# Performance work log

Measured on AMD Instinct MI355X. Metric: run time of the kernel, lower is better.

Reference implementation:

```python
import jax, jax.numpy as jnp
import numpy as np

B, IN, OUT = 256, 1024, 1024

def leaky_clamp(x, lo, hi, slope):
    return jnp.where(x < lo, lo + slope * (x - lo),
           jnp.where(x > hi, hi + slope * (x - hi), x))

def setup_inputs() -> dict:
    key = jax.random.key(0)
    kx, kw = jax.random.split(key)
    x = jax.random.normal(kx, (B, IN), dtype=jnp.float32)
    # xavier_normal for (out,in): std = sqrt(2/(in+out))
    std = np.sqrt(2.0 / (IN + OUT)).astype(np.float32)
    weight = jax.random.normal(kw, (OUT, IN), dtype=jnp.float32) * std
    log_tau = jnp.zeros((), dtype=jnp.float32)
    return {"x": x, "weight": weight, "log_tau": log_tau}

def reference(x, weight, log_tau):
    # actual_weight = leaky_clamp(weight, 0, 1, 0.1)
    aw = leaky_clamp(weight, 0.0, 1.0, 0.1)          # (OUT, IN)
    tau = jnp.exp(log_tau)                            # scalar
    z = x[:, None, :] * aw[None, :, :]                # (B, OUT, IN)
    p = jax.nn.softmax(tau * z, axis=-1)              # (B, OUT, IN)
    s = jnp.sum(p * z, axis=-1)                       # (B, OUT)
    return s
```

## Files before the change

kernel.cpp:

```cpp
#include <hip/hip_runtime.h>

#define BB   256
#define IN_  1024
#define OUTN 1024

#define TB  16
#define TO  16
#define KC  256
#define PAD 4

#define LOG2E 1.4426950408889634f

__device__ __forceinline__ float leaky_clamp01(float v) {
    float lo  = fminf(v, 0.0f);
    float hi  = fmaxf(v - 1.0f, 0.0f);
    float mid = fminf(fmaxf(v, 0.0f), 1.0f);
    return fmaf(0.1f, lo + hi, mid);
}

__global__ __launch_bounds__(256, 4)
void esm_fused_kernel(const float* __restrict__ x,
                      const float* __restrict__ w,
                      const float* __restrict__ log_tau,
                      float* __restrict__ out) {
    __shared__ float xs[TB][KC + PAD];
    __shared__ float wls[TO][KC + PAD];

    const int tid = threadIdx.x;
    const int bid = blockIdx.x;
    const int bt = bid >> 6;
    const int ot = bid & 63;
    const int b0 = bt * TB;
    const int o0 = ot * TO;

    const float scale = __expf(log_tau[0]) * LOG2E;

    const int tx = tid & 15;
    const int ty = tid >> 4;

    float da = 0.f, db = 0.f, na = 0.f, nb = 0.f;

    for (int s = 0; s < IN_ / KC; ++s) {
        const int i0 = s * KC;
        __syncthreads();
        #pragma unroll
        for (int t = 0; t < 4; ++t) {
            const int f   = tid + t * 256;
            const int row = f >> 6;
            const int i4  = (f & 63) << 2;
            const float4 v = *(const float4*)&x[(size_t)(b0 + row) * IN_ + i0 + i4];
            float4 xv;
            xv.x = v.x * scale; xv.y = v.y * scale;
            xv.z = v.z * scale; xv.w = v.w * scale;
            *(float4*)&xs[row][i4] = xv;
            const float4 u = *(const float4*)&w[(size_t)(o0 + row) * IN_ + i0 + i4];
            float4 wv;
            wv.x = leaky_clamp01(u.x); wv.y = leaky_clamp01(u.y);
            wv.z = leaky_clamp01(u.z); wv.w = leaky_clamp01(u.w);
            *(float4*)&wls[row][i4] = wv;
        }
        __syncthreads();

        #pragma unroll 4
        for (int i = 0; i < KC; i += 4) {
            const float4 xa = *(const float4*)&xs[ty][i];
            const float4 wa = *(const float4*)&wls[tx][i];
            const float t0 = xa.x * wa.x;
            const float t1 = xa.y * wa.y;
            const float t2 = xa.z * wa.z;
            const float t3 = xa.w * wa.w;
            const float e0 = __builtin_amdgcn_exp2f(t0);
            const float e1 = __builtin_amdgcn_exp2f(t1);
            const float e2 = __builtin_amdgcn_exp2f(t2);
            const float e3 = __builtin_amdgcn_exp2f(t3);
            da += e0; db += e1;
            na = fmaf(e0, t0, na); nb = fmaf(e1, t1, nb);
            da += e2; db += e3;
            na = fmaf(e2, t2, na); nb = fmaf(e3, t3, nb);
        }
    }

    out[(size_t)(b0 + ty) * OUTN + o0 + tx] = (na + nb) / ((da + db) * scale);
}

extern "C" void kernel_launch(void* const* d_in, const int* in_sizes, int n_in,
                              void* d_out, int out_size, void* d_ws, size_t ws_size,
                              hipStream_t stream) {
    const float* x  = (const float*)d_in[0];
    const float* w  = (const float*)d_in[1];
    const float* lt = (const float*)d_in[2];
    float* out = (float*)d_out;

    esm_fused_kernel<<<(BB / TB) * (OUTN / TO), 256, 0, stream>>>(x, w, lt, out);
}
```

Baseline: 94.27 us.

## Prefetch next K-chunk into registers, use packed FP32 math and med3 clamp

The x and weight tiles for the next K chunk are loaded into registers while the current chunk is computed, so global load latency overlaps the exp-heavy inner loop. The inner loop's multiply, add and FMA now use v_pk_mul/add/fma_f32 inline asm to halve VALU instruction count. The leaky clamp is rewritten as a single fmed3 and barriers become raw s_waitcnt+s_barrier. This raises register pressure from the prefetch buffers, and the inline asm may limit compiler scheduling. The transcendental exp2 throughput likely still bounds the loop.

```diff
diff --git a/kernel.cpp b/kernel.cpp
--- a/kernel.cpp
+++ b/kernel.cpp
@@ -7,15 +7,30 @@
 #define TB  16
 #define TO  16
 #define KC  256
+#define NS  (IN_ / KC)
 #define PAD 4
 
 #define LOG2E 1.4426950408889634f
 
+typedef float v2f __attribute__((ext_vector_type(2)));
+typedef float v4f __attribute__((ext_vector_type(4)));
+
+__device__ __forceinline__ v2f pk_mul(v2f a, v2f b) {
+    v2f d; asm("v_pk_mul_f32 %0, %1, %2" : "=v"(d) : "v"(a), "v"(b)); return d;
+}
+__device__ __forceinline__ v2f pk_add(v2f a, v2f b) {
+    v2f d; asm("v_pk_add_f32 %0, %1, %2" : "=v"(d) : "v"(a), "v"(b)); return d;
+}
+__device__ __forceinline__ v2f pk_fma(v2f a, v2f b, v2f c) {
+    v2f d; asm("v_pk_fma_f32 %0, %1, %2, %3" : "=v"(d) : "v"(a), "v"(b), "v"(c)); return d;
+}
+
+__device__ __forceinline__ void lds_barrier() {
+    asm volatile("s_waitcnt lgkmcnt(0)\n\ts_barrier" ::: "memory");
+}
+
 __device__ __forceinline__ float leaky_clamp01(float v) {
-    float lo  = fminf(v, 0.0f);
-    float hi  = fmaxf(v - 1.0f, 0.0f);
-    float mid = fminf(fmaxf(v, 0.0f), 1.0f);
-    return fmaf(0.1f, lo + hi, mid);
+    return __builtin_amdgcn_fmed3f(v, 0.1f * v, fmaf(0.1f, v, 0.9f));
 }
 
 __global__ __launch_bounds__(256, 4)
@@ -38,49 +53,73 @@
     const int tx = tid & 15;
     const int ty = tid >> 4;
 
-    float da = 0.f, db = 0.f, na = 0.f, nb = 0.f;
+    const int srow = tid >> 6;
+    const int si4  = (tid & 63) << 2;
 
-    for (int s = 0; s < IN_ / KC; ++s) {
-        const int i0 = s * KC;
-        __syncthreads();
+    float4 rx[4], rw[4];
+    #pragma unroll
+    for (int t = 0; t < 4; ++t) {
+        const int row = srow + t * 4;
+        rx[t] = *(const float4*)&x[(size_t)(b0 + row) * IN_ + si4];
+        rw[t] = *(const float4*)&w[(size_t)(o0 + row) * IN_ + si4];
+    }
+
+    v2f d0 = {0.f, 0.f}, d1 = {0.f, 0.f};
+    v2f n0 = {0.f, 0.f}, n1 = {0.f, 0.f};
+
+    #pragma unroll
+    for (int s = 0; s < NS; ++s) {
+        if (s) lds_barrier();
         #pragma unroll
         for (int t = 0; t < 4; ++t) {
-            const int f   = tid + t * 256;
-            const int row = f >> 6;
-            const int i4  = (f & 63) << 2;
-            const float4 v = *(const float4*)&x[(size_t)(b0 + row) * IN_ + i0 + i4];
-            float4 xv;
-            xv.x = v.x * scale; xv.y = v.y * scale;
-            xv.z = v.z * scale; xv.w = v.w * scale;
-            *(float4*)&xs[row][i4] = xv;
-            const float4 u = *(const float4*)&w[(size_t)(o0 + row) * IN_ + i0 + i4];
-            float4 wv;
-            wv.x = leaky_clamp01(u.x); wv.y = leaky_clamp01(u.y);
-            wv.z = leaky_clamp01(u.z); wv.w = leaky_clamp01(u.w);
-            *(float4*)&wls[row][i4] = wv;
+            const int row = srow + t * 4;
+            const float4 xv = rx[t];
+            float4 xo;
+            xo.x = xv.x * scale; xo.y = xv.y * scale;
+            xo.z = xv.z * scale; xo.w = xv.w * scale;
+            *(float4*)&xs[row][si4] = xo;
+            const float4 wv = rw[t];
+            float4 wo;
+            wo.x = leaky_clamp01(wv.x); wo.y = leaky_clamp01(wv.y);
+            wo.z = leaky_clamp01(wv.z); wo.w = leaky_clamp01(wv.w);
+            *(float4*)&wls[row][si4] = wo;
         }
-        __syncthreads();
+        if (s + 1 < NS) {
+            const int i0n = (s + 1) * KC;
+            #pragma unroll
+            for (int t = 0; t < 4; ++t) {
+                const int row = srow + t * 4;
+                rx[t] = *(const float4*)&x[(size_t)(b0 + row) * IN_ + i0n + si4];
+                rw[t] = *(const float4*)&w[(size_t)(o0 + row) * IN_ + i0n + si4];
+            }
+        }
+        lds_barrier();
 
         #pragma unroll 4
         for (int i = 0; i < KC; i += 4) {
-            const float4 xa = *(const float4*)&xs[ty][i];
-            const float4 wa = *(const float4*)&wls[tx][i];
-            const float t0 = xa.x * wa.x;
-            const float t1 = xa.y * wa.y;
-            const float t2 = xa.z * wa.z;
-            const float t3 = xa.w * wa.w;
-            const float e0 = __builtin_amdgcn_exp2f(t0);
-            const float e1 = __builtin_amdgcn_exp2f(t1);
-            const float e2 = __builtin_amdgcn_exp2f(t2);
-            const float e3 = __builtin_amdgcn_exp2f(t3);
-            da += e0; db += e1;
-            na = fmaf(e0, t0, na); nb = fmaf(e1, t1, nb);
-            da += e2; db += e3;
-            na = fmaf(e2, t2, na); nb = fmaf(e3, t3, nb);
+            const v4f xa = *(const v4f*)&xs[ty][i];
+            const v4f wa = *(const v4f*)&wls[tx][i];
+            const v2f xl = __builtin_shufflevector(xa, xa, 0, 1);
+            const v2f xh = __builtin_shufflevector(xa, xa, 2, 3);
+            const v2f wl = __builtin_shufflevector(wa, wa, 0, 1);
+            const v2f wh = __builtin_shufflevector(wa, wa, 2, 3);
+            const v2f t0 = pk_mul(xl, wl);
+            const v2f t1 = pk_mul(xh, wh);
+            v2f e0, e1;
+            e0.x = __builtin_amdgcn_exp2f(t0.x);
+            e0.y = __builtin_amdgcn_exp2f(t0.y);
+            e1.x = __builtin_amdgcn_exp2f(t1.x);
+            e1.y = __builtin_amdgcn_exp2f(t1.y);
+            d0 = pk_add(d0, e0);
+            d1 = pk_add(d1, e1);
+            n0 = pk_fma(e0, t0, n0);
+            n1 = pk_fma(e1, t1, n1);
         }
     }
 
-    out[(size_t)(b0 + ty) * OUTN + o0 + tx] = (na + nb) / ((da + db) * scale);
+    const float dsum = (d0.x + d0.y) + (d1.x + d1.y);
+    const float nsum = (n0.x + n0.y) + (n1.x + n1.y);
+    out[(size_t)(b0 + ty) * OUTN + o0 + tx] = nsum / (dsum * scale);
 }
 
 extern "C" void kernel_launch(void* const* d_in, const int* in_sizes, int n_in,
```

Result: no change. 93.76 us (-0.5%).

## Use 64x64 register-tiled blocks with split-K partials and a finalize kernel

Applied to the files above, without the earlier changes.

Each thread now computes a 4x4 register tile from 64x64 output tiles. This cuts LDS loads per exp from two float4 reads per element group to eight per sixteen groups. The IN dimension is split eight ways across blocks, which writes partial denominators and numerators to workspace, and a second kernel reduces them and divides. The leaky clamp becomes a single med3, and the scale is folded into the weights. The cost is an extra launch and 16 MB of partial traffic, plus higher register pressure under the 2-wave launch bound.

```diff
diff --git a/kernel.cpp b/kernel.cpp
--- a/kernel.cpp
+++ b/kernel.cpp
@@ -4,83 +4,120 @@
 #define IN_  1024
 #define OUTN 1024
 
-#define TB  16
-#define TO  16
-#define KC  256
-#define PAD 4
+#define TBb  64
+#define TOo  64
+#define NI   8
+#define KC   (IN_ / NI)
+#define LSTR (KC + 4)
 
 #define LOG2E 1.4426950408889634f
 
 __device__ __forceinline__ float leaky_clamp01(float v) {
-    float lo  = fminf(v, 0.0f);
-    float hi  = fmaxf(v - 1.0f, 0.0f);
-    float mid = fminf(fmaxf(v, 0.0f), 1.0f);
-    return fmaf(0.1f, lo + hi, mid);
+    return __builtin_amdgcn_fmed3f(v, 0.1f * v, fmaf(0.1f, v, 0.9f));
 }
 
-__global__ __launch_bounds__(256, 4)
-void esm_fused_kernel(const float* __restrict__ x,
-                      const float* __restrict__ w,
-                      const float* __restrict__ log_tau,
-                      float* __restrict__ out) {
-    __shared__ float xs[TB][KC + PAD];
-    __shared__ float wls[TO][KC + PAD];
+__global__ __launch_bounds__(256, 2)
+void esm_partial_kernel(const float* __restrict__ x,
+                        const float* __restrict__ w,
+                        const float* __restrict__ log_tau,
+                        float* __restrict__ dpart,
+                        float* __restrict__ npart) {
+    __shared__ float xs[TBb][LSTR];
+    __shared__ float wls[TOo][LSTR];
 
     const int tid = threadIdx.x;
     const int bid = blockIdx.x;
-    const int bt = bid >> 6;
-    const int ot = bid & 63;
-    const int b0 = bt * TB;
-    const int o0 = ot * TO;
+    const int ic = bid & 7;
+    const int ot = (bid >> 3) & 15;
+    const int bt = bid >> 7;
+    const int b0 = bt * TBb;
+    const int o0 = ot * TOo;
+    const int i0 = ic * KC;
 
     const float scale = __expf(log_tau[0]) * LOG2E;
+
+    const int srow = tid >> 5;
+    const int si4  = (tid & 31) << 2;
+    #pragma unroll
+    for (int t = 0; t < 8; ++t) {
+        const int row = srow + 8 * t;
+        *(float4*)&xs[row][si4] =
+            *(const float4*)&x[(size_t)(b0 + row) * IN_ + i0 + si4];
+        const float4 v = *(const float4*)&w[(size_t)(o0 + row) * IN_ + i0 + si4];
+        float4 wo;
+        wo.x = leaky_clamp01(v.x) * scale;
+        wo.y = leaky_clamp01(v.y) * scale;
+        wo.z = leaky_clamp01(v.z) * scale;
+        wo.w = leaky_clamp01(v.w) * scale;
+        *(float4*)&wls[row][si4] = wo;
+    }
+    __syncthreads();
 
     const int tx = tid & 15;
     const int ty = tid >> 4;
 
-    float da = 0.f, db = 0.f, na = 0.f, nb = 0.f;
+    float dacc[4][4] = {{0.f}};
+    float nacc[4][4] = {{0.f}};
 
-    for (int s = 0; s < IN_ / KC; ++s) {
-        const int i0 = s * KC;
-        __syncthreads();
+    for (int i = 0; i < KC; i += 4) {
+        float4 xv[4], wv[4];
         #pragma unroll
-        for (int t = 0; t < 4; ++t) {
-            const int f   = tid + t * 256;
-            const int row = f >> 6;
-            const int i4  = (f & 63) << 2;
-            const float4 v = *(const float4*)&x[(size_t)(b0 + row) * IN_ + i0 + i4];
-            float4 xv;
-            xv.x = v.x * scale; xv.y = v.y * scale;
-            xv.z = v.z * scale; xv.w = v.w * scale;
-            *(float4*)&xs[row][i4] = xv;
-            const float4 u = *(const float4*)&w[(size_t)(o0 + row) * IN_ + i0 + i4];
-            float4 wv;
-            wv.x = leaky_clamp01(u.x); wv.y = leaky_clamp01(u.y);
-            wv.z = leaky_clamp01(u.z); wv.w = leaky_clamp01(u.w);
-            *(float4*)&wls[row][i4] = wv;
-        }
-        __syncthreads();
-
-        #pragma unroll 4
-        for (int i = 0; i < KC; i += 4) {
-            const float4 xa = *(const float4*)&xs[ty][i];
-            const float4 wa = *(const float4*)&wls[tx][i];
-            const float t0 = xa.x * wa.x;
-            const float t1 = xa.y * wa.y;
-            const float t2 = xa.z * wa.z;
-            const float t3 = xa.w * wa.w;
-            const float e0 = __builtin_amdgcn_exp2f(t0);
-            const float e1 = __builtin_amdgcn_exp2f(t1);
-            const float e2 = __builtin_amdgcn_exp2f(t2);
-            const float e3 = __builtin_amdgcn_exp2f(t3);
-            da += e0; db += e1;
-            na = fmaf(e0, t0, na); nb = fmaf(e1, t1, nb);
-            da += e2; db += e3;
-            na = fmaf(e2, t2, na); nb = fmaf(e3, t3, nb);
+        for (int a = 0; a < 4; ++a) xv[a] = *(const float4*)&xs[ty + 16 * a][i];
+        #pragma unroll
+        for (int c = 0; c < 4; ++c) wv[c] = *(const float4*)&wls[tx + 16 * c][i];
+        #pragma unroll
+        for (int a = 0; a < 4; ++a) {
+            #pragma unroll
+            for (int c = 0; c < 4; ++c) {
+                const float t0 = xv[a].x * wv[c].x;
+                const float t1 = xv[a].y * wv[c].y;
+                const float t2 = xv[a].z * wv[c].z;
+                const float t3 = xv[a].w * wv[c].w;
+                const float e0 = __builtin_amdgcn_exp2f(t0);
+                const float e1 = __builtin_amdgcn_exp2f(t1);
+                const float e2 = __builtin_amdgcn_exp2f(t2);
+                const float e3 = __builtin_amdgcn_exp2f(t3);
+                dacc[a][c] += ((e0 + e1) + (e2 + e3));
+                nacc[a][c] = fmaf(e0, t0, fmaf(e1, t1,
+                             fmaf(e2, t2, fmaf(e3, t3, nacc[a][c]))));
+            }
         }
     }
 
-    out[(size_t)(b0 + ty) * OUTN + o0 + tx] = (na + nb) / ((da + db) * scale);
+    float* __restrict__ dp = dpart + (size_t)ic * BB * OUTN;
+    float* __restrict__ np = npart + (size_t)ic * BB * OUTN;
+    #pragma unroll
+    for (int a = 0; a < 4; ++a) {
+        const size_t rb = (size_t)(b0 + ty + 16 * a) * OUTN + o0 + tx;
+        #pragma unroll
+        for (int c = 0; c < 4; ++c) {
+            dp[rb + 16 * c] = dacc[a][c];
+            np[rb + 16 * c] = nacc[a][c];
+        }
+    }
+}
+
+__global__ __launch_bounds__(256)
+void esm_finalize_kernel(const float* __restrict__ dpart,
+                         const float* __restrict__ npart,
+                         const float* __restrict__ log_tau,
+                         float* __restrict__ out) {
+    const int idx = blockIdx.x * 256 + threadIdx.x;
+    const float inv = 1.0f / (__expf(log_tau[0]) * LOG2E);
+    float4 ds = {0.f, 0.f, 0.f, 0.f}, ns = {0.f, 0.f, 0.f, 0.f};
+    #pragma unroll
+    for (int ic = 0; ic < NI; ++ic) {
+        const float4 d4 = ((const float4*)dpart)[(size_t)ic * (BB * OUTN / 4) + idx];
+        const float4 n4 = ((const float4*)npart)[(size_t)ic * (BB * OUTN / 4) + idx];
+        ds.x += d4.x; ds.y += d4.y; ds.z += d4.z; ds.w += d4.w;
+        ns.x += n4.x; ns.y += n4.y; ns.z += n4.z; ns.w += n4.w;
+    }
+    float4 o4;
+    o4.x = ns.x / ds.x * inv;
+    o4.y = ns.y / ds.y * inv;
+    o4.z = ns.z / ds.z * inv;
+    o4.w = ns.w / ds.w * inv;
+    ((float4*)out)[idx] = o4;
 }
 
 extern "C" void kernel_launch(void* const* d_in, const int* in_sizes, int n_in,
@@ -91,5 +128,11 @@
     const float* lt = (const float*)d_in[2];
     float* out = (float*)d_out;
 
-    esm_fused_kernel<<<(BB / TB) * (OUTN / TO), 256, 0, stream>>>(x, w, lt, out);
+    float* dpart = (float*)d_ws;
+    float* npart = dpart + (size_t)NI * BB * OUTN;
+
+    esm_partial_kernel<<<(BB / TBb) * (OUTN / TOo) * NI, 256, 0, stream>>>(
+        x, w, lt, dpart, npart);
+    esm_finalize_kernel<<<(BB * OUTN) / 1024, 256, 0, stream>>>(
+        dpart, npart, lt, out);
 }
```

New measurement: 101.0 us. 1.07x slower.
